# Kernel optimization log

Hardware: AMD Instinct MI355X
Metric: run time of the kernel (lower is better)

Reference implementation:

```python
import jax, jax.numpy as jnp
import numpy as np

N_NODES = 50000
N_EDGES = 800000
D = 128
EPS = 1e-5


def _glorot(key, shape):
    fan_in, fan_out = shape[0], shape[1] if len(shape) > 1 else 1
    s = jnp.sqrt(2.0 / (fan_in + fan_out))
    return jax.random.normal(key, shape, dtype=jnp.float32) * s


def setup_inputs() -> dict:
    key = jax.random.key(0)
    ks = jax.random.split(key, 16)
    h = jax.random.normal(ks[0], (N_NODES, D), dtype=jnp.float32)
    e = jax.random.normal(ks[1], (N_EDGES, D), dtype=jnp.float32)
    src = jax.random.randint(ks[2], (N_EDGES,), 0, N_NODES, dtype=jnp.int32)
    dst = jax.random.randint(ks[3], (N_EDGES,), 0, N_NODES, dtype=jnp.int32)
    # weights stored [in, out] (i.e. torch W.T); biases [out]
    W_fc = _glorot(ks[4], (D, D))
    W_fce = _glorot(ks[5], (D, D))
    a_attn = _glorot(ks[6], (3 * D,))      # attn_fc weight (out=1)
    a_attn_e = _glorot(ks[7], (3 * D,))    # attn_fc_e weight
    W_B1 = _glorot(ks[8], (D, D)); b_B1 = jnp.zeros((D,), jnp.float32)
    W_B2 = _glorot(ks[9], (D, D)); b_B2 = jnp.zeros((D,), jnp.float32)
    W_B3 = _glorot(ks[10], (D, D)); b_B3 = jnp.zeros((D,), jnp.float32)
    W_mix = _glorot(ks[11], (2 * D, D)); b_mix = jnp.zeros((D,), jnp.float32)
    ln_g = jnp.ones((D,), jnp.float32); ln_b = jnp.zeros((D,), jnp.float32)
    return dict(h=h, e=e, src=src, dst=dst, W_fc=W_fc, W_fce=W_fce,
                a_attn=a_attn, a_attn_e=a_attn_e,
                W_B1=W_B1, b_B1=b_B1, W_B2=W_B2, b_B2=b_B2,
                W_B3=W_B3, b_B3=b_B3, W_mix=W_mix, b_mix=b_mix,
                ln_g=ln_g, ln_b=ln_b)


def _segment_softmax(scores, seg, num_segments):
    # scores: [E]; softmax over edges sharing the same destination node
    m = jax.ops.segment_max(scores, seg, num_segments=num_segments)
    ex = jnp.exp(scores - m[seg])
    denom = jax.ops.segment_sum(ex, seg, num_segments=num_segments)
    return ex / denom[seg]


def _gat_side(z, z_e, s, d_idx, a_attn, a_attn_e, W_mix, b_mix, n):
    # attn_fc(concat[z_src, z_e, z_dst]) split into three small matvecs
    d = z.shape[1]
    zs1, zs2, zs3 = z @ a_attn[:d], z_e @ a_attn[d:2 * d], z @ a_attn[2 * d:]
    ze1, ze2, ze3 = z @ a_attn_e[:d], z_e @ a_attn_e[d:2 * d], z @ a_attn_e[2 * d:]
    score = jax.nn.leaky_relu(zs1[s] + zs2 + zs3[d_idx], negative_slope=0.01)
    score_e = jax.nn.leaky_relu(ze1[s] + ze2 + ze3[d_idx], negative_slope=0.01)
    alpha = _segment_softmax(score, d_idx, n)
    alpha_e = _segment_softmax(score_e, d_idx, n)
    h_agg = jax.ops.segment_sum(alpha[:, None] * z[s], d_idx, num_segments=n)
    he_agg = jax.ops.segment_sum(alpha_e[:, None] * z_e, d_idx, num_segments=n)
    return jnp.concatenate([h_agg, he_agg], axis=-1) @ W_mix + b_mix


def reference(h, e, src, dst, W_fc, W_fce, a_attn, a_attn_e,
              W_B1, b_B1, W_B2, b_B2, W_B3, b_B3, W_mix, b_mix, ln_g, ln_b):
    n = h.shape[0]
    B1h = h @ W_B1 + b_B1
    B2h = h @ W_B2 + b_B2
    B3e = e @ W_B3 + b_B3
    # forward-graph edge update: e_ji = relu(B1h[u] + B2h[v] + B3e) + e (residual)
    e_ji = jax.nn.relu(B1h[src] + B2h[dst] + B3e) + e
    z = h @ W_fc
    z_e = e_ji @ W_fce
    # forward graph aggregates into dst; reverse graph into src
    h_f = _gat_side(z, z_e, src, dst, a_attn, a_attn_e, W_mix, b_mix, n)
    h_r = _gat_side(z, z_e, dst, src, a_attn, a_attn_e, W_mix, b_mix, n)
    h_out = h_f + h_r
    # LayerNorm (batch_norm=False branch)
    mu = jnp.mean(h_out, axis=-1, keepdims=True)
    var = jnp.var(h_out, axis=-1, keepdims=True)
    h_out = (h_out - mu) / jnp.sqrt(var + EPS) * ln_g + ln_b
    h_out = jax.nn.relu(h_out) + h  # residual; dropout=0 (eval)
    return h_out, e_ji
```

## Files before the change

### kernel.cpp

```cpp
#include <hip/hip_runtime.h>
#include <hip/hip_bf16.h>


typedef _Float16 f16x8 __attribute__((ext_vector_type(8)));
typedef float f32x4 __attribute__((ext_vector_type(4)));

__device__ inline float lrelu(float x) { return x > 0.f ? x : 0.01f * x; }

__device__ inline unsigned short f2bf(float f) {
  unsigned u = __float_as_uint(f);
  unsigned r = (u + 0x7FFFu + ((u >> 16) & 1u)) >> 16;
  return (unsigned short)r;
}
__device__ inline float bf2f(unsigned short us) {
  return __uint_as_float(((unsigned)us) << 16);
}

__global__ void k_combine(const float* __restrict__ Wfc, const float* __restrict__ Wfce,
                          const float* __restrict__ Wmix, const float* __restrict__ aat,
                          const float* __restrict__ aate, float* __restrict__ Mc,
                          float* __restrict__ cvec) {
  int b = blockIdx.x, j = threadIdx.x;
  if (b < 256) {
    const float* Arow;
    const float* Wm;
    if (b < 128) { Arow = Wfc + b * 128; Wm = Wmix; }
    else         { Arow = Wfce + (b - 128) * 128; Wm = Wmix + 128 * 128; }
    float acc = 0.f;
    for (int t = 0; t < 128; ++t) acc += Arow[t] * Wm[t * 128 + j];
    Mc[b * 128 + j] = acc;
  } else {
    int idx = b - 256;
    const float* W; const float* a;
    switch (idx) {
      case 0: W = Wfc;  a = aat;        break;
      case 1: W = Wfce; a = aat + 128;  break;
      case 2: W = Wfc;  a = aat + 256;  break;
      case 3: W = Wfc;  a = aate;       break;
      case 4: W = Wfce; a = aate + 128; break;
      default: W = Wfc; a = aate + 256; break;
    }
    float acc = 0.f;
    for (int t = 0; t < 128; ++t) acc += W[j * 128 + t] * a[t];
    cvec[idx * 128 + j] = acc;
  }
}

__global__ __launch_bounds__(256) void k_wt_f16(const float* __restrict__ W,
                                                _Float16* __restrict__ WT) {
  int idx = blockIdx.x * 256 + threadIdx.x;
  int c = idx >> 7, k = idx & 127;
  WT[idx] = (_Float16)W[k * 128 + c];
}

__global__ __launch_bounds__(256) void k_gemm_dual(const float* __restrict__ A,
                                                   const float* __restrict__ W1,
                                                   const float* __restrict__ b1v,
                                                   const float* __restrict__ W2,
                                                   const float* __restrict__ b2v,
                                                   const float* __restrict__ cvec,
                                                   float* __restrict__ out1,
                                                   float* __restrict__ out2,
                                                   unsigned short* __restrict__ hh,
                                                   float* __restrict__ zs1, float* __restrict__ zs3,
                                                   float* __restrict__ ze1, float* __restrict__ ze3,
                                                   int M) {
  __shared__ float Als[64][128];
  int tid = threadIdx.x;
  int cg = tid & 31, rg = tid >> 5;
  long mbase = (long)blockIdx.x * 64;
  float acc1[8][4] = {}, acc2[8][4] = {};
#pragma unroll
  for (int it = 0; it < 8; ++it) {
    int idx = tid + it * 256;
    int r = idx >> 5, cv = idx & 31;
    long m = mbase + r;
    float4 v = make_float4(0.f, 0.f, 0.f, 0.f);
    if (m < M) v = *(const float4*)&A[m * 128 + 4 * cv];
    *(float4*)&Als[r][4 * cv] = v;
  }
  __syncthreads();
  for (int k = 0; k < 128; ++k) {
    float4 w1 = *(const float4*)&W1[k * 128 + 4 * cg];
    float4 w2 = *(const float4*)&W2[k * 128 + 4 * cg];
#pragma unroll
    for (int rr = 0; rr < 8; ++rr) {
      float a = Als[rg * 8 + rr][k];
      acc1[rr][0] += a * w1.x; acc1[rr][1] += a * w1.y;
      acc1[rr][2] += a * w1.z; acc1[rr][3] += a * w1.w;
      acc2[rr][0] += a * w2.x; acc2[rr][1] += a * w2.y;
      acc2[rr][2] += a * w2.z; acc2[rr][3] += a * w2.w;
    }
  }
  float4 bb1 = *(const float4*)&b1v[4 * cg];
  float4 bb2 = *(const float4*)&b2v[4 * cg];
  float4 c1v = *(const float4*)&cvec[4 * cg];
  float4 c3v = *(const float4*)&cvec[256 + 4 * cg];
  float4 e1v = *(const float4*)&cvec[384 + 4 * cg];
  float4 e3v = *(const float4*)&cvec[640 + 4 * cg];
#pragma unroll
  for (int rr = 0; rr < 8; ++rr) {
    int rl = rg * 8 + rr;
    long m = mbase + rl;
    bool valid = (m < M);
    float a0 = Als[rl][4 * cg + 0], a1 = Als[rl][4 * cg + 1];
    float a2 = Als[rl][4 * cg + 2], a3 = Als[rl][4 * cg + 3];
    if (valid) {
      float4 o1, o2;
      o1.x = acc1[rr][0] + bb1.x; o1.y = acc1[rr][1] + bb1.y;
      o1.z = acc1[rr][2] + bb1.z; o1.w = acc1[rr][3] + bb1.w;
      o2.x = acc2[rr][0] + bb2.x; o2.y = acc2[rr][1] + bb2.y;
      o2.z = acc2[rr][2] + bb2.z; o2.w = acc2[rr][3] + bb2.w;
      *(float4*)&out1[m * 128 + 4 * cg] = o1;
      *(float4*)&out2[m * 128 + 4 * cg] = o2;
      uint2 hp;
      hp.x = (unsigned)f2bf(a0) | ((unsigned)f2bf(a1) << 16);
      hp.y = (unsigned)f2bf(a2) | ((unsigned)f2bf(a3) << 16);
      *(uint2*)&hh[m * 128 + 4 * cg] = hp;
    }
    float p1 = a0 * c1v.x + a1 * c1v.y + a2 * c1v.z + a3 * c1v.w;
    float p3 = a0 * c3v.x + a1 * c3v.y + a2 * c3v.z + a3 * c3v.w;
    float q1 = a0 * e1v.x + a1 * e1v.y + a2 * e1v.z + a3 * e1v.w;
    float q3 = a0 * e3v.x + a1 * e3v.y + a2 * e3v.z + a3 * e3v.w;
#pragma unroll
    for (int mk = 1; mk < 32; mk <<= 1) {
      p1 += __shfl_xor(p1, mk); p3 += __shfl_xor(p3, mk);
      q1 += __shfl_xor(q1, mk); q3 += __shfl_xor(q3, mk);
    }
    if (valid && cg == 0) { zs1[m] = p1; zs3[m] = p3; ze1[m] = q1; ze3[m] = q3; }
  }
}

__global__ __launch_bounds__(256) void k_edge(const float* __restrict__ e,
                                              const _Float16* __restrict__ WT,
                                              const float* __restrict__ bias,
                                              const float* __restrict__ B1h,
                                              const float* __restrict__ B2h,
                                              const int* __restrict__ src, const int* __restrict__ dst,
                                              const float* __restrict__ cs2, const float* __restrict__ ce2,
                                              float* __restrict__ eout, unsigned short* __restrict__ ejh,
                                              float* __restrict__ zs2, float* __restrict__ ze2, int M) {
  __shared__ float Als[64][132];
  int tid = threadIdx.x;
  int lane = tid & 63, w = tid >> 6;
  int kgrp = lane >> 4, sub = lane & 15;
  long mbase = (long)blockIdx.x * 64;
#pragma unroll
  for (int it = 0; it < 8; ++it) {
    int idx = tid + it * 256;
    int r = idx >> 5, cv = idx & 31;
    long m = mbase + r;
    float4 v = make_float4(0.f, 0.f, 0.f, 0.f);
    if (m < M) v = *(const float4*)&e[m * 128 + 4 * cv];
    *(float4*)&Als[r][4 * cv] = v;
  }
  __syncthreads();

  int arow = w * 16 + sub;
  f16x8 afr[4];
#pragma unroll
  for (int ks = 0; ks < 4; ++ks) {
    float4 u0 = *(const float4*)&Als[arow][ks * 32 + kgrp * 8];
    float4 u1 = *(const float4*)&Als[arow][ks * 32 + kgrp * 8 + 4];
    f16x8 a;
    a[0] = (_Float16)u0.x; a[1] = (_Float16)u0.y; a[2] = (_Float16)u0.z; a[3] = (_Float16)u0.w;
    a[4] = (_Float16)u1.x; a[5] = (_Float16)u1.y; a[6] = (_Float16)u1.z; a[7] = (_Float16)u1.w;
    afr[ks] = a;
  }

  f32x4 acc[8];
#pragma unroll
  for (int t = 0; t < 8; ++t) acc[t] = (f32x4){0.f, 0.f, 0.f, 0.f};
#pragma unroll
  for (int ks = 0; ks < 4; ++ks)
#pragma unroll
    for (int t = 0; t < 8; ++t) {
      f16x8 b = *(const f16x8*)&WT[(t * 16 + sub) * 128 + ks * 32 + kgrp * 8];
      acc[t] = __builtin_amdgcn_mfma_f32_16x16x32_f16(afr[ks], b, acc[t], 0, 0, 0);
    }

  float bb[8], cs[8], ce[8];
#pragma unroll
  for (int t = 0; t < 8; ++t) {
    int c = t * 16 + sub;
    bb[t] = bias[c];
    cs[t] = cs2[c];
    ce[t] = ce2[c];
  }

#pragma unroll
  for (int r = 0; r < 4; ++r) {
    int rl = w * 16 + kgrp * 4 + r;
    long m = mbase + rl;
    float ps = 0.f, pe = 0.f;
    if (m < M) {
      int s = src[m], dv = dst[m];
      const float* b1p = B1h + (long)s * 128;
      const float* b2p = B2h + (long)dv * 128;
#pragma unroll
      for (int t = 0; t < 8; ++t) {
        int c = t * 16 + sub;
        float o = fmaxf(acc[t][r] + bb[t] + b1p[c] + b2p[c], 0.f) + Als[rl][c];
        eout[m * 128 + c] = o;
        ejh[m * 128 + c] = f2bf(o);
        ps += o * cs[t];
        pe += o * ce[t];
      }
    }
#pragma unroll
    for (int mk = 1; mk < 16; mk <<= 1) {
      ps += __shfl_xor(ps, mk);
      pe += __shfl_xor(pe, mk);
    }
    if (m < M && sub == 0) { zs2[m] = ps; ze2[m] = pe; }
  }
}

__global__ void k_hist(const int* __restrict__ src, const int* __restrict__ dst,
                       int* __restrict__ cntf, int* __restrict__ cntr, int E) {
  int e = blockIdx.x * 256 + threadIdx.x;
  if (e < E) {
    atomicAdd(&cntf[dst[e]], 1);
    atomicAdd(&cntr[src[e]], 1);
  }
}

__global__ __launch_bounds__(1024) void k_scan(const int* __restrict__ cntf,
                                               const int* __restrict__ cntr,
                                               int* __restrict__ offf, int* __restrict__ offr, int n) {
  __shared__ int part[1024];
  int tid = threadIdx.x;
  for (int pass = 0; pass < 2; ++pass) {
    const int* cnt = pass ? cntr : cntf;
    int* off = pass ? offr : offf;
    int per = (n + 1023) >> 10;
    int beg = tid * per; if (beg > n) beg = n;
    int end = beg + per; if (end > n) end = n;
    int s = 0;
    for (int i = beg; i < end; ++i) s += cnt[i];
    part[tid] = s;
    __syncthreads();
    for (int o = 1; o < 1024; o <<= 1) {
      int vv = (tid >= o) ? part[tid - o] : 0;
      __syncthreads();
      part[tid] += vv;
      __syncthreads();
    }
    int run = tid ? part[tid - 1] : 0;
    for (int i = beg; i < end; ++i) { off[i] = run; run += cnt[i]; }
    if (tid == 1023) off[n] = part[1023];
    __syncthreads();
  }
}

__global__ void k_fill(const int* __restrict__ src, const int* __restrict__ dst,
                       const int* __restrict__ offf, const int* __restrict__ offr,
                       int* __restrict__ curf, int* __restrict__ curr,
                       int* __restrict__ eidf, int* __restrict__ eidr, int E) {
  int e = blockIdx.x * 256 + threadIdx.x;
  if (e >= E) return;
  int d = dst[e];
  int p = atomicAdd(&curf[d], 1);
  eidf[offf[d] + p] = e;
  int s = src[e];
  p = atomicAdd(&curr[s], 1);
  eidr[offr[s] + p] = e;
}

__global__ void k_scores(const int* __restrict__ src, const int* __restrict__ dst,
                         const int* __restrict__ eidf, const int* __restrict__ eidr,
                         const float* __restrict__ zs1, const float* __restrict__ zs2,
                         const float* __restrict__ zs3, const float* __restrict__ ze1,
                         const float* __restrict__ ze2, const float* __restrict__ ze3,
                         float* __restrict__ sf, float* __restrict__ sef,
                         float* __restrict__ sr, float* __restrict__ ser, int E) {
  int p = blockIdx.x * 256 + threadIdx.x;
  if (p >= E) return;
  {
    int e = eidf[p];
    int s = src[e], d = dst[e];
    float z2 = zs2[e], ze2v = ze2[e];
    sf[p] = lrelu(zs1[s] + z2 + zs3[d]);
    sef[p] = lrelu(ze1[s] + ze2v + ze3[d]);
  }
  {
    int e = eidr[p];
    int s = src[e], d = dst[e];
    float z2 = zs2[e], ze2v = ze2[e];
    sr[p] = lrelu(zs1[d] + z2 + zs3[s]);
    ser[p] = lrelu(ze1[d] + ze2v + ze3[s]);
  }
}

__device__ inline float wred_max64(float v) {
#pragma unroll
  for (int mk = 32; mk; mk >>= 1) v = fmaxf(v, __shfl_xor(v, mk));
  return v;
}
__device__ inline float wred_sum64(float v) {
#pragma unroll
  for (int mk = 32; mk; mk >>= 1) v += __shfl_xor(v, mk);
  return v;
}

__global__ __launch_bounds__(256) void k_agg4(const int* __restrict__ offf, const int* __restrict__ eidf,
                                              const int* __restrict__ offr, const int* __restrict__ eidr,
                                              const int* __restrict__ src, const int* __restrict__ dst,
                                              const float* __restrict__ sf, const float* __restrict__ sef,
                                              const float* __restrict__ sr, const float* __restrict__ ser,
                                              const unsigned short* __restrict__ hh,
                                              const unsigned short* __restrict__ ejh,
                                              float* __restrict__ agg2, int n) {
  int gw = blockIdx.x * 4 + (threadIdx.x >> 6);
  int lane = threadIdx.x & 63;
  if (gw >= 2 * n) return;
  int dir = gw & 1;
  int v = gw >> 1;
  const int* off = dir ? offr : offf;
  const int* eid = dir ? eidr : eidf;
  const float* sc  = dir ? sr  : sf;
  const float* sce = dir ? ser : sef;
  const int* nbr = dir ? dst : src;
  int s0 = off[v], s1 = off[v + 1];
  float m1 = -1e30f, m2 = -1e30f;
  for (int i = s0 + lane; i < s1; i += 64) {
    m1 = fmaxf(m1, sc[i]);
    m2 = fmaxf(m2, sce[i]);
  }
  m1 = wred_max64(m1); m2 = wred_max64(m2);
  float d1 = 0.f, d2 = 0.f;
  for (int i = s0 + lane; i < s1; i += 64) {
    d1 += __expf(sc[i] - m1);
    d2 += __expf(sce[i] - m2);
  }
  d1 = wred_sum64(d1); d2 = wred_sum64(d2);
  float i1 = (s1 > s0) ? 1.f / d1 : 0.f;
  float i2 = (s1 > s0) ? 1.f / d2 : 0.f;
  float aH0 = 0.f, aH1 = 0.f, aE0 = 0.f, aE1 = 0.f;
  for (int i = s0; i < s1; ++i) {
    int e_ = eid[i];
    int nb = nbr[e_];
    float w1 = __expf(sc[i] - m1) * i1;
    float w2 = __expf(sce[i] - m2) * i2;
    unsigned hp = *(const unsigned*)&hh[(long)nb * 128 + 2 * lane];
    unsigned ep = *(const unsigned*)&ejh[(long)e_ * 128 + 2 * lane];
    aH0 += w1 * bf2f((unsigned short)(hp & 0xFFFFu));
    aH1 += w1 * bf2f((unsigned short)(hp >> 16));
    aE0 += w2 * bf2f((unsigned short)(ep & 0xFFFFu));
    aE1 += w2 * bf2f((unsigned short)(ep >> 16));
  }
  float* dstp = agg2 + ((long)dir * n + v) * 256;
  dstp[2 * lane] = aH0;
  dstp[2 * lane + 1] = aH1;
  dstp[128 + 2 * lane] = aE0;
  dstp[128 + 2 * lane + 1] = aE1;
}

__global__ __launch_bounds__(256) void k_mix_ln(const float* __restrict__ A,
                                                const float* __restrict__ W,
                                                const float* __restrict__ bias,
                                                const float* __restrict__ h,
                                                const float* __restrict__ g,
                                                const float* __restrict__ bn,
                                                float* __restrict__ outp, int M) {
  __shared__ float Als[64][128];
  int tid = threadIdx.x;
  int cg = tid & 31, rg = tid >> 5;
  long mbase = (long)blockIdx.x * 64;
  const float* A2 = A + (long)M * 256;
  float acc[8][4] = {};
  for (int kc = 0; kc < 256; kc += 128) {
    __syncthreads();
#pragma unroll
    for (int it = 0; it < 8; ++it) {
      int idx = tid + it * 256;
      int r = idx >> 5, cv = idx & 31;
      long m = mbase + r;
      float4 v = make_float4(0.f, 0.f, 0.f, 0.f);
      if (m < M) {
        float4 v1 = *(const float4*)&A[m * 256 + kc + 4 * cv];
        float4 v2 = *(const float4*)&A2[m * 256 + kc + 4 * cv];
        v = make_float4(v1.x + v2.x, v1.y + v2.y, v1.z + v2.z, v1.w + v2.w);
      }
      *(float4*)&Als[r][4 * cv] = v;
    }
    __syncthreads();
    for (int k = 0; k < 128; ++k) {
      float4 w = *(const float4*)&W[(kc + k) * 128 + 4 * cg];
#pragma unroll
      for (int rr = 0; rr < 8; ++rr) {
        float a = Als[rg * 8 + rr][k];
        acc[rr][0] += a * w.x; acc[rr][1] += a * w.y;
        acc[rr][2] += a * w.z; acc[rr][3] += a * w.w;
      }
    }
  }
  float4 bb = *(const float4*)&bias[4 * cg];
  float4 gv = *(const float4*)&g[4 * cg];
  float4 bv = *(const float4*)&bn[4 * cg];
#pragma unroll
  for (int rr = 0; rr < 8; ++rr) {
    long m = mbase + rg * 8 + rr;
    float x0 = acc[rr][0] + 2.f * bb.x;
    float x1 = acc[rr][1] + 2.f * bb.y;
    float x2 = acc[rr][2] + 2.f * bb.z;
    float x3 = acc[rr][3] + 2.f * bb.w;
    float s = x0 + x1 + x2 + x3;
    float q = x0 * x0 + x1 * x1 + x2 * x2 + x3 * x3;
#pragma unroll
    for (int mk = 1; mk < 32; mk <<= 1) {
      s += __shfl_xor(s, mk);
      q += __shfl_xor(q, mk);
    }
    float mu = s * (1.f / 128.f);
    float var = q * (1.f / 128.f) - mu * mu;
    float rstd = rsqrtf(var + 1e-5f);
    if (m < M) {
      float4 hv = *(const float4*)&h[m * 128 + 4 * cg];
      float4 o;
      o.x = fmaxf((x0 - mu) * rstd * gv.x + bv.x, 0.f) + hv.x;
      o.y = fmaxf((x1 - mu) * rstd * gv.y + bv.y, 0.f) + hv.y;
      o.z = fmaxf((x2 - mu) * rstd * gv.z + bv.z, 0.f) + hv.z;
      o.w = fmaxf((x3 - mu) * rstd * gv.w + bv.w, 0.f) + hv.w;
      *(float4*)&outp[m * 128 + 4 * cg] = o;
    }
  }
}

extern "C" void kernel_launch(void* const* d_in, const int* in_sizes, int n_in,
                              void* d_out, int out_size, void* d_ws, size_t ws_size,
                              hipStream_t stream) {
  const float* h = (const float*)d_in[0];
  const float* e = (const float*)d_in[1];
  const int* src = (const int*)d_in[2];
  const int* dst = (const int*)d_in[3];
  const float* Wfc = (const float*)d_in[4];
  const float* Wfce = (const float*)d_in[5];
  const float* aat = (const float*)d_in[6];
  const float* aate = (const float*)d_in[7];
  const float* WB1 = (const float*)d_in[8];
  const float* bB1 = (const float*)d_in[9];
  const float* WB2 = (const float*)d_in[10];
  const float* bB2 = (const float*)d_in[11];
  const float* WB3 = (const float*)d_in[12];
  const float* bB3 = (const float*)d_in[13];
  const float* Wmix = (const float*)d_in[14];
  const float* bmix = (const float*)d_in[15];
  const float* lng = (const float*)d_in[16];
  const float* lnb = (const float*)d_in[17];
  int n = in_sizes[0] / 128;
  int E = in_sizes[1] / 128;

  float* hout = (float*)d_out;
  float* eout = (float*)d_out + (size_t)n * 128;

  char* w = (char*)d_ws;
  auto alloc = [&](size_t bytes) {
    void* p = w;
    w += (bytes + 255) / 256 * 256;
    return p;
  };
  float* B1h = (float*)alloc((size_t)n * 128 * 4);
  float* B2h = (float*)alloc((size_t)n * 128 * 4);
  float* agg2 = (float*)alloc((size_t)n * 512 * 4);
  float* zs1 = (float*)alloc((size_t)n * 4);
  float* zs3 = (float*)alloc((size_t)n * 4);
  float* ze1 = (float*)alloc((size_t)n * 4);
  float* ze3 = (float*)alloc((size_t)n * 4);
  float* zs2 = (float*)alloc((size_t)E * 4);
  float* ze2 = (float*)alloc((size_t)E * 4);
  float* sf = (float*)alloc((size_t)E * 4);
  float* sef = (float*)alloc((size_t)E * 4);
  float* sr = (float*)alloc((size_t)E * 4);
  float* ser = (float*)alloc((size_t)E * 4);
  float* Mc = (float*)alloc(256 * 128 * 4);
  float* cvec = (float*)alloc(768 * 4);
  _Float16* WT = (_Float16*)alloc(128 * 128 * 2);
  int* offf = (int*)alloc((size_t)(n + 1) * 4);
  int* offr = (int*)alloc((size_t)(n + 1) * 4);
  size_t curpad = ((size_t)n * 4 + 255) / 256 * 256;
  int* curf = (int*)alloc((size_t)n * 4);
  int* curr = (int*)alloc((size_t)n * 4);
  int* eidf = (int*)alloc((size_t)E * 4);
  int* eidr = (int*)alloc((size_t)E * 4);
  unsigned short* ejh = (unsigned short*)alloc((size_t)E * 128 * 2);
  unsigned short* hh = (unsigned short*)alloc((size_t)n * 128 * 2);

  hipMemsetAsync(curf, 0, curpad * 2, stream);

  k_combine<<<262, 128, 0, stream>>>(Wfc, Wfce, Wmix, aat, aate, Mc, cvec);
  k_wt_f16<<<64, 256, 0, stream>>>(WB3, WT);
  k_gemm_dual<<<(n + 63) / 64, 256, 0, stream>>>(h, WB1, bB1, WB2, bB2, cvec, B1h, B2h, hh,
                                                 zs1, zs3, ze1, ze3, n);
  k_hist<<<(E + 255) / 256, 256, 0, stream>>>(src, dst, curf, curr, E);
  k_scan<<<1, 1024, 0, stream>>>(curf, curr, offf, offr, n);
  hipMemsetAsync(curf, 0, curpad * 2, stream);
  k_fill<<<(E + 255) / 256, 256, 0, stream>>>(src, dst, offf, offr, curf, curr, eidf, eidr, E);
  k_edge<<<(E + 63) / 64, 256, 0, stream>>>(e, WT, bB3, B1h, B2h, src, dst,
                                            cvec + 128, cvec + 512, eout, ejh, zs2, ze2, E);
  k_scores<<<(E + 255) / 256, 256, 0, stream>>>(src, dst, eidf, eidr, zs1, zs2, zs3, ze1, ze2, ze3,
                                                sf, sef, sr, ser, E);
  k_agg4<<<(2 * n + 3) / 4, 256, 0, stream>>>(offf, eidf, offr, eidr, src, dst, sf, sef, sr, ser,
                                              hh, ejh, agg2, n);
  k_mix_ln<<<(n + 63) / 64, 256, 0, stream>>>(agg2, Mc, bmix, h, lng, lnb, hout, n);
}
```

Measured before the change: 1.275 ms.

## Write bf16 edge features in CSR order per direction for contiguous aggregation reads

The fill kernel now records each edge's position in the forward and reverse CSR orderings. The edge kernel uses these to scatter its bf16 output into two copies, one sorted by destination and one by source. The aggregation kernel can then read edge features sequentially by CSR index instead of gathering by edge id. This turns random gathers into streaming reads at the cost of writing a second 200MB bf16 array with scattered stores.

```diff
diff --git a/kernel.cpp b/kernel.cpp
--- a/kernel.cpp
+++ b/kernel.cpp
@@ -137,8 +137,11 @@
                                               const float* __restrict__ B1h,
                                               const float* __restrict__ B2h,
                                               const int* __restrict__ src, const int* __restrict__ dst,
+                                              const int* __restrict__ posf, const int* __restrict__ posr,
                                               const float* __restrict__ cs2, const float* __restrict__ ce2,
-                                              float* __restrict__ eout, unsigned short* __restrict__ ejh,
+                                              float* __restrict__ eout,
+                                              unsigned short* __restrict__ ejh_f,
+                                              unsigned short* __restrict__ ejh_r,
                                               float* __restrict__ zs2, float* __restrict__ ze2, int M) {
   __shared__ float Als[64][132];
   int tid = threadIdx.x;
@@ -195,6 +198,7 @@
     float ps = 0.f, pe = 0.f;
     if (m < M) {
       int s = src[m], dv = dst[m];
+      long pf = posf[m], pr = posr[m];
       const float* b1p = B1h + (long)s * 128;
       const float* b2p = B2h + (long)dv * 128;
 #pragma unroll
@@ -202,7 +206,9 @@
         int c = t * 16 + sub;
         float o = fmaxf(acc[t][r] + bb[t] + b1p[c] + b2p[c], 0.f) + Als[rl][c];
         eout[m * 128 + c] = o;
-        ejh[m * 128 + c] = f2bf(o);
+        unsigned short ob = f2bf(o);
+        ejh_f[pf * 128 + c] = ob;
+        ejh_r[pr * 128 + c] = ob;
         ps += o * cs[t];
         pe += o * ce[t];
       }
@@ -256,15 +262,20 @@
 __global__ void k_fill(const int* __restrict__ src, const int* __restrict__ dst,
                        const int* __restrict__ offf, const int* __restrict__ offr,
                        int* __restrict__ curf, int* __restrict__ curr,
-                       int* __restrict__ eidf, int* __restrict__ eidr, int E) {
+                       int* __restrict__ eidf, int* __restrict__ eidr,
+                       int* __restrict__ posf, int* __restrict__ posr, int E) {
   int e = blockIdx.x * 256 + threadIdx.x;
   if (e >= E) return;
   int d = dst[e];
   int p = atomicAdd(&curf[d], 1);
-  eidf[offf[d] + p] = e;
+  int qf = offf[d] + p;
+  eidf[qf] = e;
+  posf[e] = qf;
   int s = src[e];
   p = atomicAdd(&curr[s], 1);
-  eidr[offr[s] + p] = e;
+  int qr = offr[s] + p;
+  eidr[qr] = e;
+  posr[e] = qr;
 }
 
 __global__ void k_scores(const int* __restrict__ src, const int* __restrict__ dst,
@@ -303,13 +314,14 @@
   return v;
 }
 
-__global__ __launch_bounds__(256) void k_agg4(const int* __restrict__ offf, const int* __restrict__ eidf,
+__global__ __launch_bounds__(256) void k_agg5(const int* __restrict__ offf, const int* __restrict__ eidf,
                                               const int* __restrict__ offr, const int* __restrict__ eidr,
                                               const int* __restrict__ src, const int* __restrict__ dst,
                                               const float* __restrict__ sf, const float* __restrict__ sef,
                                               const float* __restrict__ sr, const float* __restrict__ ser,
                                               const unsigned short* __restrict__ hh,
-                                              const unsigned short* __restrict__ ejh,
+                                              const unsigned short* __restrict__ ejh_f,
+                                              const unsigned short* __restrict__ ejh_r,
                                               float* __restrict__ agg2, int n) {
   int gw = blockIdx.x * 4 + (threadIdx.x >> 6);
   int lane = threadIdx.x & 63;
@@ -321,6 +333,7 @@
   const float* sc  = dir ? sr  : sf;
   const float* sce = dir ? ser : sef;
   const int* nbr = dir ? dst : src;
+  const unsigned short* ejp = dir ? ejh_r : ejh_f;
   int s0 = off[v], s1 = off[v + 1];
   float m1 = -1e30f, m2 = -1e30f;
   for (int i = s0 + lane; i < s1; i += 64) {
@@ -343,7 +356,7 @@
     float w1 = __expf(sc[i] - m1) * i1;
     float w2 = __expf(sce[i] - m2) * i2;
     unsigned hp = *(const unsigned*)&hh[(long)nb * 128 + 2 * lane];
-    unsigned ep = *(const unsigned*)&ejh[(long)e_ * 128 + 2 * lane];
+    unsigned ep = *(const unsigned*)&ejp[(long)i * 128 + 2 * lane];
     aH0 += w1 * bf2f((unsigned short)(hp & 0xFFFFu));
     aH1 += w1 * bf2f((unsigned short)(hp >> 16));
     aE0 += w2 * bf2f((unsigned short)(ep & 0xFFFFu));
@@ -483,7 +496,10 @@
   int* curr = (int*)alloc((size_t)n * 4);
   int* eidf = (int*)alloc((size_t)E * 4);
   int* eidr = (int*)alloc((size_t)E * 4);
-  unsigned short* ejh = (unsigned short*)alloc((size_t)E * 128 * 2);
+  int* posf = (int*)alloc((size_t)E * 4);
+  int* posr = (int*)alloc((size_t)E * 4);
+  unsigned short* ejh_f = (unsigned short*)alloc((size_t)E * 128 * 2);
+  unsigned short* ejh_r = (unsigned short*)alloc((size_t)E * 128 * 2);
   unsigned short* hh = (unsigned short*)alloc((size_t)n * 128 * 2);
 
   hipMemsetAsync(curf, 0, curpad * 2, stream);
@@ -495,12 +511,14 @@
   k_hist<<<(E + 255) / 256, 256, 0, stream>>>(src, dst, curf, curr, E);
   k_scan<<<1, 1024, 0, stream>>>(curf, curr, offf, offr, n);
   hipMemsetAsync(curf, 0, curpad * 2, stream);
-  k_fill<<<(E + 255) / 256, 256, 0, stream>>>(src, dst, offf, offr, curf, curr, eidf, eidr, E);
-  k_edge<<<(E + 63) / 64, 256, 0, stream>>>(e, WT, bB3, B1h, B2h, src, dst,
-                                            cvec + 128, cvec + 512, eout, ejh, zs2, ze2, E);
+  k_fill<<<(E + 255) / 256, 256, 0, stream>>>(src, dst, offf, offr, curf, curr, eidf, eidr,
+                                              posf, posr, E);
+  k_edge<<<(E + 63) / 64, 256, 0, stream>>>(e, WT, bB3, B1h, B2h, src, dst, posf, posr,
+                                            cvec + 128, cvec + 512, eout, ejh_f, ejh_r,
+                                            zs2, ze2, E);
   k_scores<<<(E + 255) / 256, 256, 0, stream>>>(src, dst, eidf, eidr, zs1, zs2, zs3, ze1, ze2, ze3,
                                                 sf, sef, sr, ser, E);
-  k_agg4<<<(2 * n + 3) / 4, 256, 0, stream>>>(offf, eidf, offr, eidr, src, dst, sf, sef, sr, ser,
-                                              hh, ejh, agg2, n);
+  k_agg5<<<(2 * n + 3) / 4, 256, 0, stream>>>(offf, eidf, offr, eidr, src, dst, sf, sef, sr, ser,
+                                              hh, ejh_f, ejh_r, agg2, n);
   k_mix_ln<<<(n + 63) / 64, 256, 0, stream>>>(agg2, Mc, bmix, h, lng, lnb, hout, n);
 }
```

Result: slower. 1.391 ms (+9.1%).

## Use f16 MFMA for node-side dual GEMM and mix+LayerNorm GEMM

Applied to the files above, without the earlier changes.

Replaces the scalar FP32 FMA loops in k_gemm_dual and k_mix_ln with 16x16x32 f16 MFMA instructions, using new pre-transposed f16 copies of W_B1, W_B2 and the combined mix matrix. The aim is to cut compute time in the two node-level GEMMs, which until now ran on the vector ALUs. The cost is reduced precision (f16 inputs), two extra small transpose kernels, and output stores that are now scalar and strided per lane instead of float4. Only the node-count GEMMs are affected (50k rows), so the edge-side kernels, which likely dominate, are unchanged.

```diff
diff --git a/kernel.cpp b/kernel.cpp
--- a/kernel.cpp
+++ b/kernel.cpp
@@ -3,6 +3,7 @@
 
 
 typedef _Float16 f16x8 __attribute__((ext_vector_type(8)));
+typedef _Float16 f16x4 __attribute__((ext_vector_type(4)));
 typedef float f32x4 __attribute__((ext_vector_type(4)));
 
 __device__ inline float lrelu(float x) { return x > 0.f ? x : 0.01f * x; }
@@ -46,17 +47,32 @@
   }
 }
 
-__global__ __launch_bounds__(256) void k_wt_f16(const float* __restrict__ W,
-                                                _Float16* __restrict__ WT) {
+__global__ __launch_bounds__(256) void k_wt3(const float* __restrict__ W3,
+                                             const float* __restrict__ W1,
+                                             const float* __restrict__ W2,
+                                             _Float16* __restrict__ WT,
+                                             _Float16* __restrict__ W1T,
+                                             _Float16* __restrict__ W2T) {
   int idx = blockIdx.x * 256 + threadIdx.x;
-  int c = idx >> 7, k = idx & 127;
-  WT[idx] = (_Float16)W[k * 128 + c];
+  int which = idx >> 14;
+  int r = idx & 16383;
+  int c = r >> 7, k = r & 127;
+  const float* s = (which == 0) ? W3 : (which == 1) ? W1 : W2;
+  _Float16* d = (which == 0) ? WT : (which == 1) ? W1T : W2T;
+  d[r] = (_Float16)s[k * 128 + c];
+}
+
+__global__ __launch_bounds__(256) void k_mcT(const float* __restrict__ Mc,
+                                             _Float16* __restrict__ McT) {
+  int idx = blockIdx.x * 256 + threadIdx.x;
+  int c = idx >> 8, k = idx & 255;
+  McT[idx] = (_Float16)Mc[k * 128 + c];
 }
 
 __global__ __launch_bounds__(256) void k_gemm_dual(const float* __restrict__ A,
-                                                   const float* __restrict__ W1,
+                                                   const _Float16* __restrict__ W1T,
                                                    const float* __restrict__ b1v,
-                                                   const float* __restrict__ W2,
+                                                   const _Float16* __restrict__ W2T,
                                                    const float* __restrict__ b2v,
                                                    const float* __restrict__ cvec,
                                                    float* __restrict__ out1,
@@ -65,11 +81,11 @@
                                                    float* __restrict__ zs1, float* __restrict__ zs3,
                                                    float* __restrict__ ze1, float* __restrict__ ze3,
                                                    int M) {
-  __shared__ float Als[64][128];
+  __shared__ float Als[64][132];
   int tid = threadIdx.x;
-  int cg = tid & 31, rg = tid >> 5;
+  int lane = tid & 63, w = tid >> 6;
+  int kgrp = lane >> 4, sub = lane & 15;
   long mbase = (long)blockIdx.x * 64;
-  float acc1[8][4] = {}, acc2[8][4] = {};
 #pragma unroll
   for (int it = 0; it < 8; ++it) {
     int idx = tid + it * 256;
@@ -80,54 +96,69 @@
     *(float4*)&Als[r][4 * cv] = v;
   }
   __syncthreads();
-  for (int k = 0; k < 128; ++k) {
-    float4 w1 = *(const float4*)&W1[k * 128 + 4 * cg];
-    float4 w2 = *(const float4*)&W2[k * 128 + 4 * cg];
-#pragma unroll
-    for (int rr = 0; rr < 8; ++rr) {
-      float a = Als[rg * 8 + rr][k];
-      acc1[rr][0] += a * w1.x; acc1[rr][1] += a * w1.y;
-      acc1[rr][2] += a * w1.z; acc1[rr][3] += a * w1.w;
-      acc2[rr][0] += a * w2.x; acc2[rr][1] += a * w2.y;
-      acc2[rr][2] += a * w2.z; acc2[rr][3] += a * w2.w;
-    }
-  }
-  float4 bb1 = *(const float4*)&b1v[4 * cg];
-  float4 bb2 = *(const float4*)&b2v[4 * cg];
-  float4 c1v = *(const float4*)&cvec[4 * cg];
-  float4 c3v = *(const float4*)&cvec[256 + 4 * cg];
-  float4 e1v = *(const float4*)&cvec[384 + 4 * cg];
-  float4 e3v = *(const float4*)&cvec[640 + 4 * cg];
-#pragma unroll
-  for (int rr = 0; rr < 8; ++rr) {
-    int rl = rg * 8 + rr;
+
+  int arow = w * 16 + sub;
+  f16x8 afr[4];
+#pragma unroll
+  for (int ks = 0; ks < 4; ++ks) {
+    float4 u0 = *(const float4*)&Als[arow][ks * 32 + kgrp * 8];
+    float4 u1 = *(const float4*)&Als[arow][ks * 32 + kgrp * 8 + 4];
+    f16x8 a;
+    a[0] = (_Float16)u0.x; a[1] = (_Float16)u0.y; a[2] = (_Float16)u0.z; a[3] = (_Float16)u0.w;
+    a[4] = (_Float16)u1.x; a[5] = (_Float16)u1.y; a[6] = (_Float16)u1.z; a[7] = (_Float16)u1.w;
+    afr[ks] = a;
+  }
+
+  f32x4 acc1[8], acc2[8];
+#pragma unroll
+  for (int t = 0; t < 8; ++t) {
+    acc1[t] = (f32x4){0.f, 0.f, 0.f, 0.f};
+    acc2[t] = (f32x4){0.f, 0.f, 0.f, 0.f};
+  }
+#pragma unroll
+  for (int ks = 0; ks < 4; ++ks)
+#pragma unroll
+    for (int t = 0; t < 8; ++t) {
+      int boff = (t * 16 + sub) * 128 + ks * 32 + kgrp * 8;
+      f16x8 b1 = *(const f16x8*)&W1T[boff];
+      acc1[t] = __builtin_amdgcn_mfma_f32_16x16x32_f16(afr[ks], b1, acc1[t], 0, 0, 0);
+      f16x8 b2 = *(const f16x8*)&W2T[boff];
+      acc2[t] = __builtin_amdgcn_mfma_f32_16x16x32_f16(afr[ks], b2, acc2[t], 0, 0, 0);
+    }
+
+  float bb1[8], bb2[8];
+#pragma unroll
+  for (int t = 0; t < 8; ++t) {
+    int c = t * 16 + sub;
+    bb1[t] = b1v[c];
+    bb2[t] = b2v[c];
+  }
+
+#pragma unroll
+  for (int r = 0; r < 4; ++r) {
+    int rl = w * 16 + kgrp * 4 + r;
     long m = mbase + rl;
-    bool valid = (m < M);
-    float a0 = Als[rl][4 * cg + 0], a1 = Als[rl][4 * cg + 1];
-    float a2 = Als[rl][4 * cg + 2], a3 = Als[rl][4 * cg + 3];
-    if (valid) {
-      float4 o1, o2;
-      o1.x = acc1[rr][0] + bb1.x; o1.y = acc1[rr][1] + bb1.y;
-      o1.z = acc1[rr][2] + bb1.z; o1.w = acc1[rr][3] + bb1.w;
-      o2.x = acc2[rr][0] + bb2.x; o2.y = acc2[rr][1] + bb2.y;
-      o2.z = acc2[rr][2] + bb2.z; o2.w = acc2[rr][3] + bb2.w;
-      *(float4*)&out1[m * 128 + 4 * cg] = o1;
-      *(float4*)&out2[m * 128 + 4 * cg] = o2;
-      uint2 hp;
-      hp.x = (unsigned)f2bf(a0) | ((unsigned)f2bf(a1) << 16);
-      hp.y = (unsigned)f2bf(a2) | ((unsigned)f2bf(a3) << 16);
-      *(uint2*)&hh[m * 128 + 4 * cg] = hp;
-    }
-    float p1 = a0 * c1v.x + a1 * c1v.y + a2 * c1v.z + a3 * c1v.w;
-    float p3 = a0 * c3v.x + a1 * c3v.y + a2 * c3v.z + a3 * c3v.w;
-    float q1 = a0 * e1v.x + a1 * e1v.y + a2 * e1v.z + a3 * e1v.w;
-    float q3 = a0 * e3v.x + a1 * e3v.y + a2 * e3v.z + a3 * e3v.w;
-#pragma unroll
-    for (int mk = 1; mk < 32; mk <<= 1) {
+    float p1 = 0.f, p3 = 0.f, q1 = 0.f, q3 = 0.f;
+    if (m < M) {
+#pragma unroll
+      for (int t = 0; t < 8; ++t) {
+        int c = t * 16 + sub;
+        float a = Als[rl][c];
+        out1[m * 128 + c] = acc1[t][r] + bb1[t];
+        out2[m * 128 + c] = acc2[t][r] + bb2[t];
+        hh[m * 128 + c] = f2bf(a);
+        p1 += a * cvec[c];
+        p3 += a * cvec[256 + c];
+        q1 += a * cvec[384 + c];
+        q3 += a * cvec[640 + c];
+      }
+    }
+#pragma unroll
+    for (int mk = 1; mk < 16; mk <<= 1) {
       p1 += __shfl_xor(p1, mk); p3 += __shfl_xor(p3, mk);
       q1 += __shfl_xor(q1, mk); q3 += __shfl_xor(q3, mk);
     }
-    if (valid && cg == 0) { zs1[m] = p1; zs3[m] = p3; ze1[m] = q1; ze3[m] = q3; }
+    if (m < M && sub == 0) { zs1[m] = p1; zs3[m] = p3; ze1[m] = q1; ze3[m] = q3; }
   }
 }
 
@@ -357,58 +388,73 @@
 }
 
 __global__ __launch_bounds__(256) void k_mix_ln(const float* __restrict__ A,
-                                                const float* __restrict__ W,
+                                                const _Float16* __restrict__ McT,
                                                 const float* __restrict__ bias,
                                                 const float* __restrict__ h,
                                                 const float* __restrict__ g,
                                                 const float* __restrict__ bn,
                                                 float* __restrict__ outp, int M) {
-  __shared__ float Als[64][128];
+  __shared__ _Float16 Als[64][264];
   int tid = threadIdx.x;
-  int cg = tid & 31, rg = tid >> 5;
+  int lane = tid & 63, w = tid >> 6;
+  int kgrp = lane >> 4, sub = lane & 15;
   long mbase = (long)blockIdx.x * 64;
   const float* A2 = A + (long)M * 256;
-  float acc[8][4] = {};
-  for (int kc = 0; kc < 256; kc += 128) {
-    __syncthreads();
-#pragma unroll
-    for (int it = 0; it < 8; ++it) {
-      int idx = tid + it * 256;
-      int r = idx >> 5, cv = idx & 31;
-      long m = mbase + r;
-      float4 v = make_float4(0.f, 0.f, 0.f, 0.f);
-      if (m < M) {
-        float4 v1 = *(const float4*)&A[m * 256 + kc + 4 * cv];
-        float4 v2 = *(const float4*)&A2[m * 256 + kc + 4 * cv];
-        v = make_float4(v1.x + v2.x, v1.y + v2.y, v1.z + v2.z, v1.w + v2.w);
-      }
-      *(float4*)&Als[r][4 * cv] = v;
-    }
-    __syncthreads();
-    for (int k = 0; k < 128; ++k) {
-      float4 w = *(const float4*)&W[(kc + k) * 128 + 4 * cg];
-#pragma unroll
-      for (int rr = 0; rr < 8; ++rr) {
-        float a = Als[rg * 8 + rr][k];
-        acc[rr][0] += a * w.x; acc[rr][1] += a * w.y;
-        acc[rr][2] += a * w.z; acc[rr][3] += a * w.w;
-      }
-    }
-  }
-  float4 bb = *(const float4*)&bias[4 * cg];
-  float4 gv = *(const float4*)&g[4 * cg];
-  float4 bv = *(const float4*)&bn[4 * cg];
-#pragma unroll
-  for (int rr = 0; rr < 8; ++rr) {
-    long m = mbase + rg * 8 + rr;
-    float x0 = acc[rr][0] + 2.f * bb.x;
-    float x1 = acc[rr][1] + 2.f * bb.y;
-    float x2 = acc[rr][2] + 2.f * bb.z;
-    float x3 = acc[rr][3] + 2.f * bb.w;
-    float s = x0 + x1 + x2 + x3;
-    float q = x0 * x0 + x1 * x1 + x2 * x2 + x3 * x3;
-#pragma unroll
-    for (int mk = 1; mk < 32; mk <<= 1) {
+#pragma unroll
+  for (int it = 0; it < 16; ++it) {
+    int idx = tid + it * 256;
+    int r = idx >> 6, c4 = (idx & 63) * 4;
+    long m = mbase + r;
+    f16x4 hv = (f16x4){0, 0, 0, 0};
+    if (m < M) {
+      float4 v1 = *(const float4*)&A[m * 256 + c4];
+      float4 v2 = *(const float4*)&A2[m * 256 + c4];
+      hv[0] = (_Float16)(v1.x + v2.x);
+      hv[1] = (_Float16)(v1.y + v2.y);
+      hv[2] = (_Float16)(v1.z + v2.z);
+      hv[3] = (_Float16)(v1.w + v2.w);
+    }
+    *(f16x4*)&Als[r][c4] = hv;
+  }
+  __syncthreads();
+
+  int arow = w * 16 + sub;
+  f32x4 acc[8];
+#pragma unroll
+  for (int t = 0; t < 8; ++t) acc[t] = (f32x4){0.f, 0.f, 0.f, 0.f};
+#pragma unroll
+  for (int ks = 0; ks < 8; ++ks) {
+    f16x8 a = *(const f16x8*)&Als[arow][ks * 32 + kgrp * 8];
+#pragma unroll
+    for (int t = 0; t < 8; ++t) {
+      f16x8 b = *(const f16x8*)&McT[(t * 16 + sub) * 256 + ks * 32 + kgrp * 8];
+      acc[t] = __builtin_amdgcn_mfma_f32_16x16x32_f16(a, b, acc[t], 0, 0, 0);
+    }
+  }
+
+  float bb[8], gv[8], bv[8];
+#pragma unroll
+  for (int t = 0; t < 8; ++t) {
+    int c = t * 16 + sub;
+    bb[t] = 2.f * bias[c];
+    gv[t] = g[c];
+    bv[t] = bn[c];
+  }
+
+#pragma unroll
+  for (int r = 0; r < 4; ++r) {
+    int rl = w * 16 + kgrp * 4 + r;
+    long m = mbase + rl;
+    float x[8];
+    float s = 0.f, q = 0.f;
+#pragma unroll
+    for (int t = 0; t < 8; ++t) {
+      x[t] = acc[t][r] + bb[t];
+      s += x[t];
+      q += x[t] * x[t];
+    }
+#pragma unroll
+    for (int mk = 1; mk < 16; mk <<= 1) {
       s += __shfl_xor(s, mk);
       q += __shfl_xor(q, mk);
     }
@@ -416,13 +462,12 @@
     float var = q * (1.f / 128.f) - mu * mu;
     float rstd = rsqrtf(var + 1e-5f);
     if (m < M) {
-      float4 hv = *(const float4*)&h[m * 128 + 4 * cg];
-      float4 o;
-      o.x = fmaxf((x0 - mu) * rstd * gv.x + bv.x, 0.f) + hv.x;
-      o.y = fmaxf((x1 - mu) * rstd * gv.y + bv.y, 0.f) + hv.y;
-      o.z = fmaxf((x2 - mu) * rstd * gv.z + bv.z, 0.f) + hv.z;
-      o.w = fmaxf((x3 - mu) * rstd * gv.w + bv.w, 0.f) + hv.w;
-      *(float4*)&outp[m * 128 + 4 * cg] = o;
+      const float* hp = h + m * 128;
+#pragma unroll
+      for (int t = 0; t < 8; ++t) {
+        int c = t * 16 + sub;
+        outp[m * 128 + c] = fmaxf((x[t] - mu) * rstd * gv[t] + bv[t], 0.f) + hp[c];
+      }
     }
   }
 }
@@ -476,6 +521,9 @@
   float* Mc = (float*)alloc(256 * 128 * 4);
   float* cvec = (float*)alloc(768 * 4);
   _Float16* WT = (_Float16*)alloc(128 * 128 * 2);
+  _Float16* W1T = (_Float16*)alloc(128 * 128 * 2);
+  _Float16* W2T = (_Float16*)alloc(128 * 128 * 2);
+  _Float16* McT = (_Float16*)alloc(128 * 256 * 2);
   int* offf = (int*)alloc((size_t)(n + 1) * 4);
   int* offr = (int*)alloc((size_t)(n + 1) * 4);
   size_t curpad = ((size_t)n * 4 + 255) / 256 * 256;
@@ -489,8 +537,9 @@
   hipMemsetAsync(curf, 0, curpad * 2, stream);
 
   k_combine<<<262, 128, 0, stream>>>(Wfc, Wfce, Wmix, aat, aate, Mc, cvec);
-  k_wt_f16<<<64, 256, 0, stream>>>(WB3, WT);
-  k_gemm_dual<<<(n + 63) / 64, 256, 0, stream>>>(h, WB1, bB1, WB2, bB2, cvec, B1h, B2h, hh,
+  k_wt3<<<192, 256, 0, stream>>>(WB3, WB1, WB2, WT, W1T, W2T);
+  k_mcT<<<128, 256, 0, stream>>>(Mc, McT);
+  k_gemm_dual<<<(n + 63) / 64, 256, 0, stream>>>(h, W1T, bB1, W2T, bB2, cvec, B1h, B2h, hh,
                                                  zs1, zs3, ze1, ze3, n);
   k_hist<<<(E + 255) / 256, 256, 0, stream>>>(src, dst, curf, curr, E);
   k_scan<<<1, 1024, 0, stream>>>(curf, curr, offf, offr, n);
@@ -502,5 +551,5 @@
                                                 sf, sef, sr, ser, E);
   k_agg4<<<(2 * n + 3) / 4, 256, 0, stream>>>(offf, eidf, offr, eidr, src, dst, sf, sef, sr, ser,
                                               hh, ejh, agg2, n);
-  k_mix_ln<<<(n + 63) / 64, 256, 0, stream>>>(agg2, Mc, bmix, h, lng, lnb, hout, n);
-}
+  k_mix_ln<<<(n + 63) / 64, 256, 0, stream>>>(agg2, McT, bmix, h, lng, lnb, hout, n);
+}
```

New measurement: 1.243 ms. -2.5%, faster.
